# Optimization experiments

Hardware: AMD Instinct MI355X
Metric: run time of the kernel (lower is better)

Reference implementation:

```python
import jax, jax.numpy as jnp
import numpy as np

HEADS = 4
DIM_HEAD = 64
MAP_SIZE = 16
SCALE = DIM_HEAD ** (-0.5)


def _split_heads(x):
    # torch rearrange 'b (dim_head heads) h w -> b heads (h w) dim_head'
    B, C, H, W = x.shape
    x = x.reshape(B, DIM_HEAD, HEADS, H * W)
    return jnp.transpose(x, (0, 2, 3, 1))  # [B, heads, N, dim_head]


def _merge_heads(x, H, W):
    # torch rearrange 'b heads (h w) dim_head -> b (dim_head heads) h w'
    B, h, N, d = x.shape
    return jnp.transpose(x, (0, 3, 1, 2)).reshape(B, d * h, H, W)


def setup_inputs() -> dict:
    key = jax.random.key(0)
    ks = jax.random.split(key, 6)
    feat = jax.random.normal(ks[0], (4, 256, 96, 96), jnp.float32)
    semantic_map = jax.random.normal(ks[1], (4, 256, 16, 16), jnp.float32)
    # 1x1 conv weights, shape [out_ch, in_ch]; scaled like fan-in init
    W_feat_qv = 0.05 * jax.random.normal(ks[2], (512, 256), jnp.float32)
    W_map_qv = 0.05 * jax.random.normal(ks[3], (512, 256), jnp.float32)
    W_feat_out = 0.05 * jax.random.normal(ks[4], (256, 256), jnp.float32)
    W_map_out = 0.05 * jax.random.normal(ks[5], (256, 256), jnp.float32)
    return {
        "feat": feat,
        "semantic_map": semantic_map,
        "W_feat_qv": W_feat_qv,
        "W_map_qv": W_map_qv,
        "W_feat_out": W_feat_out,
        "W_map_out": W_map_out,
    }


def reference(feat, semantic_map, W_feat_qv, W_map_qv, W_feat_out, W_map_out):
    B, C, H, W = feat.shape
    # 1x1 convs == per-pixel channel matmuls
    fqv = jnp.einsum("oc,bchw->bohw", W_feat_qv, feat)
    feat_q, feat_v = jnp.split(fqv, 2, axis=1)
    mqv = jnp.einsum("oc,bchw->bohw", W_map_qv, semantic_map)
    map_q, map_v = jnp.split(mqv, 2, axis=1)

    feat_q, feat_v = _split_heads(feat_q), _split_heads(feat_v)  # [B,h,N,d]
    map_q, map_v = _split_heads(map_q), _split_heads(map_v)      # [B,h,M,d]

    attn = jnp.einsum("bhid,bhjd->bhij", feat_q, map_q) * SCALE  # [B,h,N,M]
    feat_map_attn = jax.nn.softmax(attn, axis=-1)  # normalize over map tokens j
    map_feat_attn = jax.nn.softmax(attn, axis=-2)  # normalize over feat tokens i

    feat_o = jnp.einsum("bhij,bhjd->bhid", feat_map_attn, map_v)   # [B,h,N,d]
    map_o = jnp.einsum("bhji,bhjd->bhid", map_feat_attn, feat_v)   # [B,h,M,d]

    feat_o = _merge_heads(feat_o, H, W)
    map_o = _merge_heads(map_o, MAP_SIZE, MAP_SIZE)

    feat_out = jnp.einsum("oc,bchw->bohw", W_feat_out, feat_o)
    map_out = jnp.einsum("oc,bchw->bohw", W_map_out, map_o)
    return feat_out, map_out
```

## Files before the change

### kernel.cpp

```cpp
#include <hip/hip_runtime.h>
#include <stdint.h>

#define DI static __device__ __forceinline__

constexpr int NTOK = 9216;
constexpr float ATT_SCALE = 0.125f;

typedef short bf16x8 __attribute__((ext_vector_type(8)));
typedef float f32x4  __attribute__((ext_vector_type(4)));

DI f32x4 mfma16(bf16x8 a, bf16x8 b, f32x4 c) {
  return __builtin_amdgcn_mfma_f32_16x16x32_bf16(a, b, c, 0, 0, 0);
}

DI float b2f(uint16_t u) { union { uint32_t i; float f; } v; v.i = ((uint32_t)u) << 16; return v.f; }
DI uint16_t f2b(float f) {
  union { float f; uint32_t i; } v; v.f = f;
  uint32_t r = (v.i + 0x7fffu + ((v.i >> 16) & 1u)) >> 16;
  return (uint16_t)r;
}

template<int DT> DI float ld1(const void* p, size_t off) {
  if constexpr (DT) return b2f(((const uint16_t*)p)[off]);
  else              return ((const float*)p)[off];
}
template<int DT> DI void st1(void* p, size_t off, float v) {
  if constexpr (DT) ((uint16_t*)p)[off] = f2b(v);
  else              ((float*)p)[off] = v;
}

DI int block_flag256(const uint32_t* __restrict__ w) {
  const float b = b2f((uint16_t)(w[threadIdx.x & 255] & 0xffffu));
  const float ab = fabsf(b);
  return (__syncthreads_count((ab > 1e-4f && ab < 0.5f) ? 1 : 0) >= 128) ? 1 : 0;
}

template<int DT>
DI void prep_w_dev(int r, const void* __restrict__ Wfqv, const void* __restrict__ Wfo,
                   uint16_t* __restrict__ WqvP, uint16_t* __restrict__ WfoP)
{
  const int c = threadIdx.x;
  if (r < 512) {
    const int sel = r >> 8, within = r & 255;
    const int h = within >> 6, d = within & 63;
    const int src = sel * 256 + d * 4 + h;
    WqvP[(size_t)r * 256 + c] = f2b(ld1<DT>(Wfqv, (size_t)src * 256 + c));
  } else {
    const int ro = r - 512;
    WfoP[(size_t)ro * 256 + c] =
        f2b(ld1<DT>(Wfo, (size_t)ro * 256 + (c & 63) * 4 + (c >> 6)));
  }
}

template<int DT>
DI void map_qv_dev(int o, int bb, const void* __restrict__ Wqv,
                   const void* __restrict__ smap,
                   uint16_t* __restrict__ MQ, uint16_t* __restrict__ MVT)
{
  const int m = threadIdx.x;
  float acc = 0.f;
  #pragma unroll 8
  for (int c = 0; c < 256; ++c)
    acc += ld1<DT>(Wqv, (size_t)o * 256 + c) *
           ld1<DT>(smap, (size_t)bb * 65536 + (size_t)c * 256 + m);
  const int oc = o & 255;
  const int h = oc & 3, d = oc >> 2;
  if (o < 256) MQ[(((size_t)bb * 4 + h) * 256 + m) * 64 + d] = f2b(acc);
  else         MVT[(((size_t)bb * 4 + h) * 64 + d) * 256 + m] = f2b(acc);
}

__global__ __launch_bounds__(256) void prep_map_k(
    const void* Wfqv, const void* Wfo, const void* Wmqv, const void* smap,
    uint16_t* WqvP, uint16_t* WfoP, uint16_t* MQ, uint16_t* MVT)
{
  const int fl = block_flag256((const uint32_t*)Wfqv);
  const int bid = blockIdx.x;
  if (bid < 768) {
    if (fl) prep_w_dev<1>(bid, Wfqv, Wfo, WqvP, WfoP);
    else    prep_w_dev<0>(bid, Wfqv, Wfo, WqvP, WfoP);
  } else {
    const int idx = bid - 768;
    if (fl) map_qv_dev<1>(idx & 511, idx >> 9, Wmqv, smap, MQ, MVT);
    else    map_qv_dev<0>(idx & 511, idx >> 9, Wmqv, smap, MQ, MVT);
  }
}

constexpr int P0 = 280;

template<int DT>
DI void gemm0_body(uint16_t* Xs, const uint16_t* __restrict__ WqvP,
                   const void* __restrict__ X,
                   uint16_t* __restrict__ FQ, uint16_t* __restrict__ FVt)
{
  const int tid = threadIdx.x;
  const int w = tid >> 6, lane = tid & 63;
  const int l = lane & 15, quad = lane >> 4;
  const int n0 = blockIdx.x * 64;
  const int bb = blockIdx.y;
  const size_t bh = (size_t)bb * 4 + w;

  {
    const int nb = (tid & 31) * 2;
    const int kg = tid >> 5;
    #pragma unroll
    for (int pass = 0; pass < 4; ++pass) {
      const int k0 = pass * 64 + kg * 8;
      union { uint16_t h[8]; uint4 u; } pk0, pk1;
      #pragma unroll
      for (int j = 0; j < 8; ++j) {
        const size_t g = ((size_t)bb * 256 + k0 + j) * NTOK + n0 + nb;
        if constexpr (DT) {
          const uint32_t v = *(const uint32_t*)((const uint16_t*)X + g);
          pk0.h[j] = (uint16_t)(v & 0xffffu);
          pk1.h[j] = (uint16_t)(v >> 16);
        } else {
          const float2 v = *(const float2*)((const float*)X + g);
          pk0.h[j] = f2b(v.x);
          pk1.h[j] = f2b(v.y);
        }
      }
      *(uint4*)(Xs + (size_t)(nb + 0) * P0 + k0) = pk0.u;
      *(uint4*)(Xs + (size_t)(nb + 1) * P0 + k0) = pk1.u;
    }
  }
  __syncthreads();

  f32x4 acc[8][4];
  #pragma unroll
  for (int a = 0; a < 8; ++a)
    #pragma unroll
    for (int b = 0; b < 4; ++b) { acc[a][b].x = 0.f; acc[a][b].y = 0.f; acc[a][b].z = 0.f; acc[a][b].w = 0.f; }

  for (int ks = 0; ks < 8; ++ks) {
    bf16x8 af[8];
    #pragma unroll
    for (int mt = 0; mt < 8; ++mt) {
      const int arow = (mt >> 2) * 256 + w * 64 + (mt & 3) * 16 + l;
      af[mt] = *(const bf16x8*)(WqvP + (size_t)arow * 256 + ks * 32 + quad * 8);
    }
    #pragma unroll
    for (int nt = 0; nt < 4; ++nt) {
      const bf16x8 bv = *(const bf16x8*)(Xs + (size_t)(nt * 16 + l) * P0 + ks * 32 + quad * 8);
      #pragma unroll
      for (int mt = 0; mt < 8; ++mt)
        acc[mt][nt] = mfma16(af[mt], bv, acc[mt][nt]);
    }
  }
  #pragma unroll
  for (int mt = 0; mt < 8; ++mt)
    #pragma unroll
    for (int nt = 0; nt < 4; ++nt) {
      const int n = n0 + nt * 16 + l;
      if (mt < 4) {
        union { uint16_t h[4]; uint2 u; } pk;
        #pragma unroll
        for (int r = 0; r < 4; ++r) pk.h[r] = f2b(acc[mt][nt][r]);
        *(uint2*)(FQ + (bh * NTOK + n) * 64 + mt * 16 + quad * 4) = pk.u;
      } else {
        const int itile = n >> 5, io = n & 31;
        #pragma unroll
        for (int r = 0; r < 4; ++r)
          FVt[(((size_t)bh * 288 + itile) * 64 + (mt - 4) * 16 + quad * 4 + r) * 32 + io] =
              f2b(acc[mt][nt][r]);
      }
    }
}
__global__ __launch_bounds__(256) void gemm0_mfma(
    const uint16_t* WqvP, const void* X, uint16_t* FQ, uint16_t* FVt,
    const void* Wfqv)
{
  __shared__ __align__(16) uint16_t Xs[64 * P0];
  const int fl = block_flag256((const uint32_t*)Wfqv);
  if (fl) gemm0_body<1>(Xs, WqvP, X, FQ, FVt);
  else    gemm0_body<0>(Xs, WqvP, X, FQ, FVt);
}

constexpr int PJ = 280;
constexpr int PI = 40;
constexpr int PO = 72;
constexpr int NGRP = 36;
constexpr int PP = 68;

__global__ __launch_bounds__(256, 3) void attn_mfma(
    const uint16_t* __restrict__ FQ, const uint16_t* __restrict__ FVt,
    const uint16_t* __restrict__ MQ, const uint16_t* __restrict__ MVT,
    uint16_t* __restrict__ FO, uint16_t* __restrict__ P)
{
  __shared__ __align__(16) uint16_t Esh[32 * PJ];
  __shared__ __align__(16) uint16_t ETsh[256 * PI];
  __shared__ __align__(16) uint16_t Osh[32 * PO];
  __shared__ float RS[4][32];
  const int tid = threadIdx.x;
  const int w = tid >> 6;
  const int lane = tid & 63;
  const int l = lane & 15, quad = lane >> 4;
  const int blk = blockIdx.x, bh = blockIdx.y;
  const uint16_t* FQh  = FQ  + (size_t)bh * NTOK * 64;
  const uint16_t* FVth = FVt + (size_t)bh * 288 * 64 * 32;
  const uint16_t* MQh  = MQ  + (size_t)bh * 256 * 64;
  const uint16_t* MVTh = MVT + (size_t)bh * 64 * 256;
  uint16_t* FOh = FO + (size_t)bh * NTOK * 64;

  bf16x8 kb[4][2];
  #pragma unroll
  for (int jt = 0; jt < 4; ++jt) {
    const int j = w * 64 + jt * 16 + l;
    kb[jt][0] = *(const bf16x8*)(MQh + (size_t)j * 64 + quad * 8);
    kb[jt][1] = *(const bf16x8*)(MQh + (size_t)j * 64 + 32 + quad * 8);
  }
  bf16x8 avr[8];
  #pragma unroll
  for (int ks = 0; ks < 8; ++ks)
    avr[ks] = *(const bf16x8*)(MVTh + (size_t)(w * 16 + l) * 256 + ks * 32 + quad * 8);

  f32x4 numacc[4][4];
  #pragma unroll
  for (int a = 0; a < 4; ++a)
    #pragma unroll
    for (int b = 0; b < 4; ++b) { numacc[a][b].x = 0.f; numacc[a][b].y = 0.f; numacc[a][b].z = 0.f; numacc[a][b].w = 0.f; }
  float csum[4] = {0.f, 0.f, 0.f, 0.f};

  for (int t = 0; t < 8; ++t) {
    const int it = blk * 8 + t;
    const int i0 = it * 32;

    bf16x8 qa[2][2];
    #pragma unroll
    for (int mt = 0; mt < 2; ++mt)
      #pragma unroll
      for (int kbi = 0; kbi < 2; ++kbi)
        qa[mt][kbi] = *(const bf16x8*)(FQh + (size_t)(i0 + mt * 16 + l) * 64 + kbi * 32 + quad * 8);

    float rsum[2][4] = {{0.f,0.f,0.f,0.f},{0.f,0.f,0.f,0.f}};
    #pragma unroll
    for (int jt = 0; jt < 4; ++jt) {
      const int j0 = w * 64 + jt * 16;
      #pragma unroll
      for (int mt = 0; mt < 2; ++mt) {
        f32x4 acc = {0.f, 0.f, 0.f, 0.f};
        acc = mfma16(qa[mt][0], kb[jt][0], acc);
        acc = mfma16(qa[mt][1], kb[jt][1], acc);
        union { uint16_t h[4]; uint2 u; } pk;
        #pragma unroll
        for (int r = 0; r < 4; ++r) {
          const float e = __expf(acc[r] * ATT_SCALE);
          rsum[mt][r] += e;
          csum[jt] += e;
          pk.h[r] = f2b(e);
          Esh[(mt * 16 + quad * 4 + r) * PJ + j0 + l] = pk.h[r];
        }
        *(uint2*)(ETsh + (size_t)(j0 + l) * PI + mt * 16 + quad * 4) = pk.u;
      }
    }
    #pragma unroll
    for (int mt = 0; mt < 2; ++mt)
      #pragma unroll
      for (int r = 0; r < 4; ++r) {
        float v = rsum[mt][r];
        v += __shfl_xor(v, 1); v += __shfl_xor(v, 2);
        v += __shfl_xor(v, 4); v += __shfl_xor(v, 8);
        if (l == 0) RS[w][mt * 16 + quad * 4 + r] = v;
      }
    __syncthreads();

    bf16x8 av[4];
    #pragma unroll
    for (int mt = 0; mt < 4; ++mt)
      av[mt] = *(const bf16x8*)(FVth + ((size_t)it * 64 + mt * 16 + l) * 32 + quad * 8);

    {
      float rinv[2];
      #pragma unroll
      for (int nt = 0; nt < 2; ++nt) {
        const int i_ = nt * 16 + l;
        rinv[nt] = 1.f / (RS[0][i_] + RS[1][i_] + RS[2][i_] + RS[3][i_]);
      }
      f32x4 oacc[2];
      oacc[0].x=0.f;oacc[0].y=0.f;oacc[0].z=0.f;oacc[0].w=0.f;
      oacc[1]=oacc[0];
      #pragma unroll
      for (int ks = 0; ks < 8; ++ks) {
        #pragma unroll
        for (int nt = 0; nt < 2; ++nt) {
          const bf16x8 bv = *(const bf16x8*)(Esh + (size_t)(nt * 16 + l) * PJ + ks * 32 + quad * 8);
          oacc[nt] = mfma16(avr[ks], bv, oacc[nt]);
        }
      }
      #pragma unroll
      for (int nt = 0; nt < 2; ++nt) {
        union { uint16_t h[4]; uint2 u; } pk;
        #pragma unroll
        for (int r = 0; r < 4; ++r) pk.h[r] = f2b(oacc[nt][r] * rinv[nt]);
        *(uint2*)(Osh + (nt * 16 + l) * PO + w * 16 + quad * 4) = pk.u;
      }
    }

    #pragma unroll
    for (int mt = 0; mt < 4; ++mt) {
      #pragma unroll
      for (int nt2 = 0; nt2 < 4; ++nt2) {
        const bf16x8 bv = *(const bf16x8*)(ETsh + (size_t)(w * 64 + nt2 * 16 + l) * PI + quad * 8);
        numacc[mt][nt2] = mfma16(av[mt], bv, numacc[mt][nt2]);
      }
    }
    __syncthreads();

    {
      const int ti = tid >> 3, c = tid & 7;
      *(uint4*)(FOh + (size_t)(i0 + ti) * 64 + c * 8) =
          *(const uint4*)(Osh + ti * PO + c * 8);
    }
  }

  uint16_t* Pb = P + ((size_t)bh * NGRP + blk) * 256 * PP;
  #pragma unroll
  for (int mt = 0; mt < 4; ++mt)
    #pragma unroll
    for (int nt2 = 0; nt2 < 4; ++nt2) {
      const int j = w * 64 + nt2 * 16 + l;
      union { uint16_t h[4]; uint2 u; } pk;
      #pragma unroll
      for (int r = 0; r < 4; ++r) pk.h[r] = f2b(numacc[mt][nt2][r]);
      *(uint2*)(Pb + (size_t)j * PP + mt * 16 + quad * 4) = pk.u;
    }
  #pragma unroll
  for (int jt = 0; jt < 4; ++jt) {
    float v = csum[jt];
    v += __shfl_xor(v, 16); v += __shfl_xor(v, 32);
    if (quad == 0) Pb[(size_t)(w * 64 + jt * 16 + l) * PP + 64] = f2b(v);
  }
}

template<int DT>
DI void gemm1_dev(int gidx, const uint16_t* __restrict__ WfoP,
                  const uint16_t* __restrict__ FO, void* __restrict__ out)
{
  const int tid = threadIdx.x;
  const int w = tid >> 6, lane = tid & 63;
  const int l = lane & 15, quad = lane >> 4;
  const int n0 = (gidx % 36) * 256;
  const int o0 = ((gidx / 36) & 3) * 64;
  const int bb = gidx / 144;

  f32x4 acc[4][4];
  #pragma unroll
  for (int a = 0; a < 4; ++a)
    #pragma unroll
    for (int b = 0; b < 4; ++b) { acc[a][b].x = 0.f; acc[a][b].y = 0.f; acc[a][b].z = 0.f; acc[a][b].w = 0.f; }

  #pragma unroll
  for (int ks = 0; ks < 8; ++ks) {
    const int h2 = ks >> 1;
    const int doff = (ks & 1) * 32 + quad * 8;
    bf16x8 af[4];
    #pragma unroll
    for (int mt = 0; mt < 4; ++mt)
      af[mt] = *(const bf16x8*)(WfoP + (size_t)(o0 + mt * 16 + l) * 256 + ks * 32 + quad * 8);
    #pragma unroll
    for (int nt = 0; nt < 4; ++nt) {
      const int n = n0 + w * 64 + nt * 16 + l;
      const bf16x8 bv = *(const bf16x8*)(FO + ((size_t)(bb * 4 + h2) * NTOK + n) * 64 + doff);
      #pragma unroll
      for (int mt = 0; mt < 4; ++mt)
        acc[mt][nt] = mfma16(af[mt], bv, acc[mt][nt]);
    }
  }
  #pragma unroll
  for (int mt = 0; mt < 4; ++mt)
    #pragma unroll
    for (int nt = 0; nt < 4; ++nt) {
      const int n = n0 + w * 64 + nt * 16 + l;
      #pragma unroll
      for (int r = 0; r < 4; ++r)
        st1<DT>(out, ((size_t)bb * 256 + o0 + mt * 16 + quad * 4 + r) * NTOK + n,
                acc[mt][nt][r]);
    }
}

DI void reduce_dev(int bid, const uint16_t* __restrict__ P, uint16_t* __restrict__ MO)
{
  const int idx = bid * 256 + threadIdx.x;
  const int d = idx & 63;
  const int j = (idx >> 6) & 255;
  const int bh = idx >> 14;
  const size_t base = (size_t)bh * NGRP * 256 * PP;
  float num = 0.f, cs = 0.f;
  #pragma unroll 6
  for (int g = 0; g < NGRP; ++g) {
    const size_t row = base + ((size_t)g * 256 + j) * PP;
    num += b2f(P[row + d]);
    cs  += b2f(P[row + 64]);
  }
  const float v = num / cs;
  const int b = bh >> 2, h = bh & 3;
  MO[((size_t)b * 256 + (d * 4 + h)) * 256 + j] = f2b(v);
}

__global__ __launch_bounds__(256) void epilogue_k(
    const uint16_t* WfoP, const uint16_t* FO, void* out,
    const uint16_t* P, uint16_t* MO, const void* Wfqv, int mode)
{
  const int bid = blockIdx.x;
  bool do_g1; int gidx;
  if (mode == 0)      { do_g1 = bid < 576; gidx = do_g1 ? bid : bid - 576; }
  else if (mode == 1) { do_g1 = true;  gidx = bid; }
  else                { do_g1 = false; gidx = bid; }
  if (do_g1) {
    const int fl = block_flag256((const uint32_t*)Wfqv);
    if (fl) gemm1_dev<1>(gidx, WfoP, FO, out);
    else    gemm1_dev<0>(gidx, WfoP, FO, out);
  } else {
    reduce_dev(gidx, P, MO);
  }
}

template<int DT>
DI void map_out_body(const void* __restrict__ Wmo, const uint16_t* __restrict__ MO,
                     void* __restrict__ out)
{
  const int o = blockIdx.x, bb = blockIdx.y, m = threadIdx.x;
  float acc = 0.f;
  #pragma unroll 8
  for (int c = 0; c < 256; ++c)
    acc += ld1<DT>(Wmo, (size_t)o * 256 + c) *
           b2f(MO[((size_t)bb * 256 + c) * 256 + m]);
  const size_t MAP_OFS = (size_t)4 * 256 * NTOK;
  st1<DT>(out, MAP_OFS + ((size_t)bb * 256 + o) * 256 + m, acc);
}
__global__ __launch_bounds__(256) void map_out_k(
    const void* Wmo, const uint16_t* MO, void* out, const void* Wfqv)
{
  const int fl = block_flag256((const uint32_t*)Wfqv);
  if (fl) map_out_body<1>(Wmo, MO, out);
  else    map_out_body<0>(Wmo, MO, out);
}

extern "C" void kernel_launch(void* const* d_in, const int* in_sizes, int n_in,
                              void* d_out, int out_size, void* d_ws, size_t ws_size,
                              hipStream_t stream) {
  (void)in_sizes; (void)n_in; (void)out_size;
  const void* feat = d_in[0];
  const void* smap = d_in[1];
  const void* Wfqv = d_in[2];
  const void* Wmqv = d_in[3];
  const void* Wfo  = d_in[4];
  const void* Wmo  = d_in[5];
  char* ws = (char*)d_ws;

  const size_t BIG = (size_t)16 * 64 * NTOK * 2;
  const size_t SML = (size_t)16 * 256 * 64 * 2;
  const size_t FQ_OFF  = 0;
  const size_t FVT_OFF = FQ_OFF + BIG;
  const size_t MQ_OFF  = FVT_OFF + BIG;
  const size_t MVT_OFF = MQ_OFF + SML;
  const size_t MO_OFF  = MVT_OFF + SML;
  const size_t WQP_OFF = MO_OFF + (size_t)4 * 256 * 256 * 2;
  const size_t WFP_OFF = WQP_OFF + (size_t)512 * 256 * 2;
  const size_t P_OFF   = WFP_OFF + (size_t)256 * 256 * 2;
  const size_t P_SIZE  = (size_t)16 * NGRP * 256 * PP * 2;
  const size_t NEED    = P_OFF + P_SIZE;

  uint16_t* FQ   = (uint16_t*)(ws + FQ_OFF);
  uint16_t* FVt  = (uint16_t*)(ws + FVT_OFF);
  uint16_t* MQ   = (uint16_t*)(ws + MQ_OFF);
  uint16_t* MVT  = (uint16_t*)(ws + MVT_OFF);
  uint16_t* MO   = (uint16_t*)(ws + MO_OFF);
  uint16_t* WqvP = (uint16_t*)(ws + WQP_OFF);
  uint16_t* WfoP = (uint16_t*)(ws + WFP_OFF);

  const bool p_in_ws = (ws_size >= NEED);
  uint16_t* P = p_in_ws ? (uint16_t*)(ws + P_OFF) : (uint16_t*)d_out;

  prep_map_k<<<dim3(2816), 256, 0, stream>>>(Wfqv, Wfo, Wmqv, smap,
                                             WqvP, WfoP, MQ, MVT);
  gemm0_mfma<<<dim3(144, 4), 256, 0, stream>>>(WqvP, feat, FQ, FVt, Wfqv);
  attn_mfma<<<dim3(NGRP, 16), 256, 0, stream>>>(FQ, FVt, MQ, MVT, FQ, P);
  if (p_in_ws) {
    epilogue_k<<<dim3(1600), 256, 0, stream>>>(WfoP, FQ, d_out, P, MO, Wfqv, 0);
  } else {
    epilogue_k<<<dim3(1024), 256, 0, stream>>>(WfoP, FQ, d_out, P, MO, Wfqv, 2);
    epilogue_k<<<dim3(576),  256, 0, stream>>>(WfoP, FQ, d_out, P, MO, Wfqv, 1);
  }
  map_out_k<<<dim3(256, 4), 256, 0, stream>>>(Wmo, MO, d_out, Wfqv);
}
```

Baseline: 291.0 us.

## Halve gemm0 tile width, raise attention groups, split column sums out of partials

The QV projection kernel now processes 32 tokens per block instead of 64, which doubles the grid and lowers per-block registers and LDS, with a 3-blocks-per-CU launch bound. The attention kernel splits the token range into 48 groups of 6 tiles instead of 36 groups of 8, giving more blocks for better CU fill at the cost of more partials to reduce. Column sums move from a padded slot inside each partial row to a separate dense array, so partial rows become unpadded 64-wide and coalesced for the reduction. The tradeoffs are a larger reduction workload and reloading the weight tile more often in gemm0.

```diff
diff --git a/kernel.cpp b/kernel.cpp
--- a/kernel.cpp
+++ b/kernel.cpp
@@ -95,16 +95,16 @@
   const int tid = threadIdx.x;
   const int w = tid >> 6, lane = tid & 63;
   const int l = lane & 15, quad = lane >> 4;
-  const int n0 = blockIdx.x * 64;
+  const int n0 = blockIdx.x * 32;
   const int bb = blockIdx.y;
   const size_t bh = (size_t)bb * 4 + w;
 
   {
-    const int nb = (tid & 31) * 2;
-    const int kg = tid >> 5;
-    #pragma unroll
-    for (int pass = 0; pass < 4; ++pass) {
-      const int k0 = pass * 64 + kg * 8;
+    const int nb = (tid & 15) * 2;
+    const int kg = tid >> 4;
+    #pragma unroll
+    for (int pass = 0; pass < 2; ++pass) {
+      const int k0 = pass * 128 + kg * 8;
       union { uint16_t h[8]; uint4 u; } pk0, pk1;
       #pragma unroll
       for (int j = 0; j < 8; ++j) {
@@ -125,51 +125,60 @@
   }
   __syncthreads();
 
-  f32x4 acc[8][4];
-  #pragma unroll
-  for (int a = 0; a < 8; ++a)
-    #pragma unroll
-    for (int b = 0; b < 4; ++b) { acc[a][b].x = 0.f; acc[a][b].y = 0.f; acc[a][b].z = 0.f; acc[a][b].w = 0.f; }
+  f32x4 acc[2][4][2];
+  #pragma unroll
+  for (int s = 0; s < 2; ++s)
+    #pragma unroll
+    for (int a = 0; a < 4; ++a)
+      #pragma unroll
+      for (int b = 0; b < 2; ++b) { acc[s][a][b].x = 0.f; acc[s][a][b].y = 0.f; acc[s][a][b].z = 0.f; acc[s][a][b].w = 0.f; }
 
   for (int ks = 0; ks < 8; ++ks) {
-    bf16x8 af[8];
-    #pragma unroll
-    for (int mt = 0; mt < 8; ++mt) {
-      const int arow = (mt >> 2) * 256 + w * 64 + (mt & 3) * 16 + l;
-      af[mt] = *(const bf16x8*)(WqvP + (size_t)arow * 256 + ks * 32 + quad * 8);
-    }
-    #pragma unroll
-    for (int nt = 0; nt < 4; ++nt) {
-      const bf16x8 bv = *(const bf16x8*)(Xs + (size_t)(nt * 16 + l) * P0 + ks * 32 + quad * 8);
-      #pragma unroll
-      for (int mt = 0; mt < 8; ++mt)
-        acc[mt][nt] = mfma16(af[mt], bv, acc[mt][nt]);
-    }
-  }
-  #pragma unroll
-  for (int mt = 0; mt < 8; ++mt)
-    #pragma unroll
-    for (int nt = 0; nt < 4; ++nt) {
+    bf16x8 bv[2];
+    #pragma unroll
+    for (int nt = 0; nt < 2; ++nt)
+      bv[nt] = *(const bf16x8*)(Xs + (size_t)(nt * 16 + l) * P0 + ks * 32 + quad * 8);
+    #pragma unroll
+    for (int s = 0; s < 2; ++s) {
+      bf16x8 af[4];
+      #pragma unroll
+      for (int mt = 0; mt < 4; ++mt) {
+        const int arow = s * 256 + w * 64 + mt * 16 + l;
+        af[mt] = *(const bf16x8*)(WqvP + (size_t)arow * 256 + ks * 32 + quad * 8);
+      }
+      #pragma unroll
+      for (int nt = 0; nt < 2; ++nt)
+        #pragma unroll
+        for (int mt = 0; mt < 4; ++mt)
+          acc[s][mt][nt] = mfma16(af[mt], bv[nt], acc[s][mt][nt]);
+    }
+  }
+  const int itile = blockIdx.x;
+  #pragma unroll
+  for (int mt = 0; mt < 4; ++mt)
+    #pragma unroll
+    for (int nt = 0; nt < 2; ++nt) {
       const int n = n0 + nt * 16 + l;
-      if (mt < 4) {
+      {
         union { uint16_t h[4]; uint2 u; } pk;
         #pragma unroll
-        for (int r = 0; r < 4; ++r) pk.h[r] = f2b(acc[mt][nt][r]);
+        for (int r = 0; r < 4; ++r) pk.h[r] = f2b(acc[0][mt][nt][r]);
         *(uint2*)(FQ + (bh * NTOK + n) * 64 + mt * 16 + quad * 4) = pk.u;
-      } else {
-        const int itile = n >> 5, io = n & 31;
+      }
+      {
+        const int io = n & 31;
         #pragma unroll
         for (int r = 0; r < 4; ++r)
-          FVt[(((size_t)bh * 288 + itile) * 64 + (mt - 4) * 16 + quad * 4 + r) * 32 + io] =
-              f2b(acc[mt][nt][r]);
-      }
-    }
-}
-__global__ __launch_bounds__(256) void gemm0_mfma(
+          FVt[(((size_t)bh * 288 + itile) * 64 + mt * 16 + quad * 4 + r) * 32 + io] =
+              f2b(acc[1][mt][nt][r]);
+      }
+    }
+}
+__global__ __launch_bounds__(256, 3) void gemm0_mfma(
     const uint16_t* WqvP, const void* X, uint16_t* FQ, uint16_t* FVt,
     const void* Wfqv)
 {
-  __shared__ __align__(16) uint16_t Xs[64 * P0];
+  __shared__ __align__(16) uint16_t Xs[32 * P0];
   const int fl = block_flag256((const uint32_t*)Wfqv);
   if (fl) gemm0_body<1>(Xs, WqvP, X, FQ, FVt);
   else    gemm0_body<0>(Xs, WqvP, X, FQ, FVt);
@@ -178,13 +187,14 @@
 constexpr int PJ = 280;
 constexpr int PI = 40;
 constexpr int PO = 72;
-constexpr int NGRP = 36;
-constexpr int PP = 68;
+constexpr int NGRP = 48;
+constexpr int TPB = 6;
 
 __global__ __launch_bounds__(256, 3) void attn_mfma(
     const uint16_t* __restrict__ FQ, const uint16_t* __restrict__ FVt,
     const uint16_t* __restrict__ MQ, const uint16_t* __restrict__ MVT,
-    uint16_t* __restrict__ FO, uint16_t* __restrict__ P)
+    uint16_t* __restrict__ FO, uint16_t* __restrict__ P,
+    uint16_t* __restrict__ CSp)
 {
   __shared__ __align__(16) uint16_t Esh[32 * PJ];
   __shared__ __align__(16) uint16_t ETsh[256 * PI];
@@ -220,8 +230,8 @@
     for (int b = 0; b < 4; ++b) { numacc[a][b].x = 0.f; numacc[a][b].y = 0.f; numacc[a][b].z = 0.f; numacc[a][b].w = 0.f; }
   float csum[4] = {0.f, 0.f, 0.f, 0.f};
 
-  for (int t = 0; t < 8; ++t) {
-    const int it = blk * 8 + t;
+  for (int t = 0; t < TPB; ++t) {
+    const int it = blk * TPB + t;
     const int i0 = it * 32;
 
     bf16x8 qa[2][2];
@@ -312,7 +322,7 @@
     }
   }
 
-  uint16_t* Pb = P + ((size_t)bh * NGRP + blk) * 256 * PP;
+  uint16_t* Pb = P + ((size_t)bh * NGRP + blk) * 256 * 64;
   #pragma unroll
   for (int mt = 0; mt < 4; ++mt)
     #pragma unroll
@@ -321,13 +331,14 @@
       union { uint16_t h[4]; uint2 u; } pk;
       #pragma unroll
       for (int r = 0; r < 4; ++r) pk.h[r] = f2b(numacc[mt][nt2][r]);
-      *(uint2*)(Pb + (size_t)j * PP + mt * 16 + quad * 4) = pk.u;
-    }
+      *(uint2*)(Pb + (size_t)j * 64 + mt * 16 + quad * 4) = pk.u;
+    }
+  uint16_t* CSb = CSp + ((size_t)bh * NGRP + blk) * 256;
   #pragma unroll
   for (int jt = 0; jt < 4; ++jt) {
     float v = csum[jt];
     v += __shfl_xor(v, 16); v += __shfl_xor(v, 32);
-    if (quad == 0) Pb[(size_t)(w * 64 + jt * 16 + l) * PP + 64] = f2b(v);
+    if (quad == 0) CSb[w * 64 + jt * 16 + l] = f2b(v);
   }
 }
 
@@ -377,19 +388,20 @@
     }
 }
 
-DI void reduce_dev(int bid, const uint16_t* __restrict__ P, uint16_t* __restrict__ MO)
+DI void reduce_dev(int bid, const uint16_t* __restrict__ P,
+                   const uint16_t* __restrict__ CSp, uint16_t* __restrict__ MO)
 {
   const int idx = bid * 256 + threadIdx.x;
   const int d = idx & 63;
   const int j = (idx >> 6) & 255;
   const int bh = idx >> 14;
-  const size_t base = (size_t)bh * NGRP * 256 * PP;
+  const size_t base = (size_t)bh * NGRP * 256 * 64;
+  const size_t cb = (size_t)bh * NGRP * 256;
   float num = 0.f, cs = 0.f;
   #pragma unroll 6
   for (int g = 0; g < NGRP; ++g) {
-    const size_t row = base + ((size_t)g * 256 + j) * PP;
-    num += b2f(P[row + d]);
-    cs  += b2f(P[row + 64]);
+    num += b2f(P[base + ((size_t)g * 256 + j) * 64 + d]);
+    cs  += b2f(CSp[cb + (size_t)g * 256 + j]);
   }
   const float v = num / cs;
   const int b = bh >> 2, h = bh & 3;
@@ -398,7 +410,8 @@
 
 __global__ __launch_bounds__(256) void epilogue_k(
     const uint16_t* WfoP, const uint16_t* FO, void* out,
-    const uint16_t* P, uint16_t* MO, const void* Wfqv, int mode)
+    const uint16_t* P, const uint16_t* CSp, uint16_t* MO,
+    const void* Wfqv, int mode)
 {
   const int bid = blockIdx.x;
   bool do_g1; int gidx;
@@ -410,7 +423,7 @@
     if (fl) gemm1_dev<1>(gidx, WfoP, FO, out);
     else    gemm1_dev<0>(gidx, WfoP, FO, out);
   } else {
-    reduce_dev(gidx, P, MO);
+    reduce_dev(gidx, P, CSp, MO);
   }
 }
 
@@ -456,8 +469,10 @@
   const size_t MO_OFF  = MVT_OFF + SML;
   const size_t WQP_OFF = MO_OFF + (size_t)4 * 256 * 256 * 2;
   const size_t WFP_OFF = WQP_OFF + (size_t)512 * 256 * 2;
-  const size_t P_OFF   = WFP_OFF + (size_t)256 * 256 * 2;
-  const size_t P_SIZE  = (size_t)16 * NGRP * 256 * PP * 2;
+  const size_t CS_OFF  = WFP_OFF + (size_t)256 * 256 * 2;
+  const size_t CS_SIZE = (size_t)16 * NGRP * 256 * 2;
+  const size_t P_OFF   = CS_OFF + CS_SIZE;
+  const size_t P_SIZE  = (size_t)16 * NGRP * 256 * 64 * 2;
   const size_t NEED    = P_OFF + P_SIZE;
 
   uint16_t* FQ   = (uint16_t*)(ws + FQ_OFF);
@@ -469,17 +484,19 @@
   uint16_t* WfoP = (uint16_t*)(ws + WFP_OFF);
 
   const bool p_in_ws = (ws_size >= NEED);
-  uint16_t* P = p_in_ws ? (uint16_t*)(ws + P_OFF) : (uint16_t*)d_out;
+  uint16_t* P   = p_in_ws ? (uint16_t*)(ws + P_OFF) : (uint16_t*)d_out;
+  uint16_t* CSp = p_in_ws ? (uint16_t*)(ws + CS_OFF)
+                          : (uint16_t*)((char*)d_out + P_SIZE);
 
   prep_map_k<<<dim3(2816), 256, 0, stream>>>(Wfqv, Wfo, Wmqv, smap,
                                              WqvP, WfoP, MQ, MVT);
-  gemm0_mfma<<<dim3(144, 4), 256, 0, stream>>>(WqvP, feat, FQ, FVt, Wfqv);
-  attn_mfma<<<dim3(NGRP, 16), 256, 0, stream>>>(FQ, FVt, MQ, MVT, FQ, P);
+  gemm0_mfma<<<dim3(288, 4), 256, 0, stream>>>(WqvP, feat, FQ, FVt, Wfqv);
+  attn_mfma<<<dim3(NGRP, 16), 256, 0, stream>>>(FQ, FVt, MQ, MVT, FQ, P, CSp);
   if (p_in_ws) {
-    epilogue_k<<<dim3(1600), 256, 0, stream>>>(WfoP, FQ, d_out, P, MO, Wfqv, 0);
+    epilogue_k<<<dim3(1600), 256, 0, stream>>>(WfoP, FQ, d_out, P, CSp, MO, Wfqv, 0);
   } else {
-    epilogue_k<<<dim3(1024), 256, 0, stream>>>(WfoP, FQ, d_out, P, MO, Wfqv, 2);
-    epilogue_k<<<dim3(576),  256, 0, stream>>>(WfoP, FQ, d_out, P, MO, Wfqv, 1);
+    epilogue_k<<<dim3(1024), 256, 0, stream>>>(WfoP, FQ, d_out, P, CSp, MO, Wfqv, 2);
+    epilogue_k<<<dim3(576),  256, 0, stream>>>(WfoP, FQ, d_out, P, CSp, MO, Wfqv, 1);
   }
   map_out_k<<<dim3(256, 4), 256, 0, stream>>>(Wmo, MO, d_out, Wfqv);
 }
```

Measured after the change: 299.8 us. +3.0%, slower.
